# Kernel tuning notes

Measured on AMD Instinct MI355X. Metric: run time of the kernel, lower is better.

Reference implementation:

```python
import jax, jax.numpy as jnp
import numpy as np


def _lstm(x, k, r, b, return_sequences=True):
    # Keras LSTM: gate order i, f, c(g), o; sigmoid recurrent activation, tanh activation.
    # x: [B,T,D], k: [D,4H], r: [H,4H], b: [4H]
    B = x.shape[0]
    H = r.shape[0]
    xk = jnp.einsum('btd,dh->bth', x, k) + b  # precompute input projections for all steps

    def step(carry, xk_t):
        h, c = carry
        z = xk_t + h @ r
        i, f, g, o = jnp.split(z, 4, axis=-1)
        i = jax.nn.sigmoid(i)
        f = jax.nn.sigmoid(f)
        g = jnp.tanh(g)
        o = jax.nn.sigmoid(o)
        c = f * c + i * g
        h = o * jnp.tanh(c)
        return (h, c), h

    h0 = jnp.zeros((B, H), x.dtype)
    (hT, _), hs = jax.lax.scan(step, (h0, jnp.zeros_like(h0)), jnp.swapaxes(xk, 0, 1))
    if return_sequences:
        return jnp.swapaxes(hs, 0, 1)  # [B,T,H]
    return hT  # [B,H]


def _bias(h):
    # Keras unit_forget_bias=True: forget-gate bias initialized to 1
    return jnp.zeros((4 * h,), jnp.float32).at[h:2 * h].set(1.0)


def setup_inputs() -> dict:
    key = jax.random.key(0)
    ks = jax.random.split(key, 20)
    B, T, D = 128, 512, 64
    s = 0.05

    def n(k, shape):
        return jax.random.normal(k, shape, jnp.float32) * s

    inp = {"x": jax.random.normal(ks[0], (B, T, D), jnp.float32)}
    lstm_dims = [(D, 640), (640, 400), (400, 256), (256, 256)]
    i = 1
    for li, (din, h) in enumerate(lstm_dims, 1):
        inp[f"k{li}"] = n(ks[i], (din, 4 * h))
        inp[f"r{li}"] = n(ks[i + 1], (h, 4 * h))
        inp[f"b{li}"] = _bias(h)
        i += 2
    dense_dims = [(256, 512), (512, 256), (256, 128), (128, 64), (64, 16), (16, 3)]
    for li, (din, dout) in enumerate(dense_dims, 1):
        inp[f"wd{li}"] = n(ks[i], (din, dout))
        inp[f"bd{li}"] = jnp.zeros((dout,), jnp.float32)
        i += 1
    return inp


def reference(x, k1, r1, b1, k2, r2, b2, k3, r3, b3, k4, r4, b4,
              wd1, bd1, wd2, bd2, wd3, bd3, wd4, bd4, wd5, bd5, wd6, bd6):
    h = _lstm(x, k1, r1, b1, return_sequences=True)
    h = _lstm(h, k2, r2, b2, return_sequences=True)
    h = _lstm(h, k3, r3, b3, return_sequences=True)
    h = _lstm(h, k4, r4, b4, return_sequences=False)  # [B, 256]
    # Dropout layers are identity at inference (Keras call without training=True)
    h = jax.nn.relu(h @ wd1 + bd1)
    h = jax.nn.relu(h @ wd2 + bd2)
    h = jax.nn.relu(h @ wd3 + bd3)
    h = jax.nn.relu(h @ wd4 + bd4)
    h = jax.nn.relu(h @ wd5 + bd5)
    logits = h @ wd6 + bd6
    return jax.nn.softmax(logits, axis=-1)  # class_count=3 branch
```

## Files before the change

### kernel.cpp

```cpp
#include <hip/hip_runtime.h>
#include <hip/hip_cooperative_groups.h>
#include <cstdint>
#include <cstddef>

namespace cg = cooperative_groups;

typedef _Float16 f16;
typedef _Float16 h8v  __attribute__((ext_vector_type(8)));
typedef float    f32x4 __attribute__((ext_vector_type(4)));

static constexpr int BATCH  = 128;
static constexpr int TSTEPS = 512;
static constexpr int NT     = 256;

static constexpr int TB1 = 80, TB2 = 100, TB3 = 32, TB4 = 32;
static constexpr int TNB   = TB1 + TB2 + TB3 + TB4;
static constexpr int NGRID = TNB + 4;

template<int RING> struct WS {
  static constexpr size_t XT  = 0;
  static constexpr size_t H1  = XT + 512ull * 128 * 64 * 2;
  static constexpr size_t H2  = H1 + (size_t)RING * 128 * 640 * 2 + 64;
  static constexpr size_t H3  = H2 + (size_t)RING * 128 * 400 * 2 + 64;
  static constexpr size_t H4  = H3 + (size_t)RING * 128 * 256 * 2 + 64;
  static constexpr size_t PK1 = H4 + (size_t)RING * 128 * 256 * 2 + 64;
  static constexpr size_t PK2 = PK1 + (size_t)TB1 * 32 * 704  * 2;
  static constexpr size_t PK3 = PK2 + (size_t)TB2 * 16 * 1056 * 2;
  static constexpr size_t PK4 = PK3 + (size_t)TB3 * 32 * 672  * 2;
  static constexpr size_t BAR = PK4 + (size_t)TB4 * 32 * 512  * 2;
  static constexpr size_t ZERO= BAR + 8192;
  static constexpr size_t END = ZERO + 163840;
};

struct KParams {
  const float *x;
  const float *k1, *r1, *b1, *k2, *r2, *b2, *k3, *r3, *b3, *k4, *r4, *b4;
  const float *wd1, *bd1, *wd2, *bd2, *wd3, *bd3, *wd4, *bd4, *wd5, *bd5, *wd6, *bd6;
  float *out;
  char *ws;
};

__device__ __forceinline__ float sigm(float v) { return 1.f / (1.f + expf(-v)); }

__device__ __forceinline__ uint64_t c_load8(const void* p) {
  return __hip_atomic_load((const uint64_t*)p, __ATOMIC_RELAXED, __HIP_MEMORY_SCOPE_AGENT);
}
__device__ __forceinline__ void c_store8(void* p, uint64_t v) {
  __hip_atomic_store((uint64_t*)p, v, __ATOMIC_RELAXED, __HIP_MEMORY_SCOPE_AGENT);
}
__device__ __forceinline__ unsigned short c_load2(const void* p) {
  return __hip_atomic_load((const unsigned short*)p, __ATOMIC_RELAXED, __HIP_MEMORY_SCOPE_AGENT);
}
__device__ __forceinline__ unsigned u_load(const unsigned* p) {
  return __hip_atomic_load(p, __ATOMIC_RELAXED, __HIP_MEMORY_SCOPE_AGENT);
}
__device__ __forceinline__ void u_store(unsigned* p, unsigned v) {
  __hip_atomic_store(p, v, __ATOMIC_RELAXED, __HIP_MEMORY_SCOPE_AGENT);
}
__device__ __forceinline__ void acq_fence() {
  __builtin_amdgcn_fence(__ATOMIC_ACQUIRE, "agent");
}

template<int NBLK>
__device__ void control_role(unsigned* U, int first, int lidx) {
  const int tid = threadIdx.x;
  int cand = 1;
  while (cand <= TSTEPS) {
    unsigned v = (tid < NBLK) ? u_load(&U[first + tid]) : 0xFFFFFFFFu;
    if (__syncthreads_and((int)(v >= (unsigned)cand))) {
      if (tid < 16) u_store(&U[512 + tid * 64 + lidx], (unsigned)cand);
      ++cand;
    }
  }
}

__device__ void prepack_layer(const float* __restrict__ gk, const float* __restrict__ gr,
                              f16* __restrict__ pack, int DIN, int H, int NJ, int KPAD,
                              int TB, int gtid, int gstr) {
  const int KREAL = DIN + H;
  const int NGC = 4 * NJ;
  const long total = (long)TB * NGC * KPAD;
  for (long e = gtid; e < total; e += gstr) {
    const int  k   = (int)(e % KPAD);
    const long r   = e / KPAD;
    const int  n   = (int)(r % NGC);
    const int  blk = (int)(r / NGC);
    const int  g   = n / NJ, jj = n % NJ;
    const int  j   = blk * NJ + jj;
    float v = 0.f;
    if (k < DIN)        v = gk[(size_t)k * 4 * H + (size_t)g * H + j];
    else if (k < KREAL) v = gr[(size_t)(k - DIN) * 4 * H + (size_t)g * H + j];
    pack[e] = (f16)v;
  }
}

#define FETCH(PP, CC) do { \
  _Pragma("unroll") \
  for (int ii_ = 0; ii_ < C; ++ii_) { \
    const int ks_ = (CC) * C + ii_; \
    if (ks_ < KS) { \
      const int k_ = ks_ * 32 + kg; \
      _Pragma("unroll") \
      for (int m_ = 0; m_ < 2; ++m_) { \
        const int bmv_ = m_ ? bm1 : bm0; \
        uint4 v_ = make_uint4(0u, 0u, 0u, 0u); \
        if constexpr (SEQM) { \
          if (k_ < DIN)        v_ = *(const uint4*)(inP + (size_t)bmv_ * DIN + k_); \
          else if (k_ < KREAL) v_ = *(const uint4*)(inH + (size_t)bmv_ * H + (k_ - DIN)); \
        } else { \
          if (k_ < DIN) { \
            const f16* p_ = inP + (size_t)bmv_ * DIN + k_; \
            if constexpr (SEQIN) { \
              ((uint64_t*)&v_)[0] = *(const uint64_t*)p_; \
              ((uint64_t*)&v_)[1] = *(const uint64_t*)(p_ + 4); \
            } else { \
              ((uint64_t*)&v_)[0] = c_load8(p_); \
              ((uint64_t*)&v_)[1] = c_load8(p_ + 4); \
            } \
          } else if (k_ < KREAL) { \
            const f16* p_ = inH + (size_t)bmv_ * H + (k_ - DIN); \
            ((uint64_t*)&v_)[0] = c_load8(p_); \
            ((uint64_t*)&v_)[1] = c_load8(p_ + 4); \
          } \
        } \
        ab[PP][ii_][m_] = v_; \
      } \
    } \
  } \
} while (0)

#define COMPUTE(PP, CC) do { \
  _Pragma("unroll") \
  for (int ii_ = 0; ii_ < C; ++ii_) { \
    const int ks_ = (CC) * C + ii_; \
    if (ks_ < KS) { \
      const int kb_ = ks_ * 32; \
      h8v bf_[NTI]; \
      _Pragma("unroll") \
      for (int nt_ = 0; nt_ < NTI; ++nt_) \
        bf_[nt_] = *(const h8v*)(wlds + (size_t)(nt_ * 16 + l15) * WROW + kb_ + kg); \
      _Pragma("unroll") \
      for (int m_ = 0; m_ < 2; ++m_) { \
        union { uint4 u; h8v v; } af_; \
        af_.u = ab[PP][ii_][m_]; \
        _Pragma("unroll") \
        for (int nt_ = 0; nt_ < NTI; ++nt_) \
          acc[m_][nt_] = __builtin_amdgcn_mfma_f32_16x16x32_f16(af_.v, bf_[nt_], acc[m_][nt_], 0, 0, 0); \
      } \
    } \
  } \
} while (0)

#define WAITOWN do { \
  if (tid == 0) { while (rcO < t) rcO = (int)u_load(&relp[LIDX]); } \
  __syncthreads(); \
} while (0)

template<int DIN, int H, int NJ, int LIDX, bool SEQIN, int RING>
__device__ void lstm_role(int blk, int bid, const f16* lo_base, f16* ownH,
                          const f16* pack, const float* __restrict__ gbias,
                          const f16* zreg, char* smem, unsigned* U) {
  constexpr bool SEQM = (RING == TSTEPS);
  constexpr int KREAL = DIN + H;
  constexpr int KS    = (KREAL + 31) / 32;
  constexpr int KPAD  = KS * 32;
  constexpr int NGC   = 4 * NJ;
  constexpr int NTI   = NGC / 16;
  constexpr int WROW  = KPAD + 8;
  constexpr int ZROW  = 132;
  constexpr int C     = 6;
  constexpr int NC    = (KS + C - 1) / C;
  constexpr int KSX   = DIN / 32;
  constexpr int CH    = KSX / C;
  static_assert(NC <= 6, "NC");
  static_assert(CH <= NC - 1, "CH");
  static_assert(NGC % 16 == 0 && (DIN % 8) == 0 && (KREAL % 8) == 0, "geom");

  const int tid  = threadIdx.x;
  const int w    = tid >> 6, lane = tid & 63;
  const int l15  = lane & 15;
  const int kg   = (lane >> 4) * 8;
  const int bm0  = w * 32 + l15;
  const int bm1  = bm0 + 16;

  f16*   wlds = (f16*)smem;
  float* z    = (float*)(smem + (size_t)NGC * WROW * 2);

  {
    const f16* src = pack + (size_t)blk * NGC * KPAD;
    constexpr int RU = KPAD / 8;
    for (int u = tid; u < NGC * RU; u += NT) {
      const int n = u / RU, k8 = u % RU;
      *(uint4*)(wlds + (size_t)n * WROW + k8 * 8) =
          *(const uint4*)(src + (size_t)n * KPAD + k8 * 8);
    }
  }
  __syncthreads();

  constexpr int JG = NJ / 4;
  const int be  = tid / JG;
  const int g4  = tid % JG;
  const bool epi = (tid < 128 * JG);
  const int j0  = blk * NJ + g4 * 4;
  f32x4 bias4[4] = {};
  if (epi) {
    #pragma unroll
    for (int g = 0; g < 4; ++g) bias4[g] = *(const f32x4*)(gbias + (size_t)g * H + j0);
  }
  float cst[4] = {0.f, 0.f, 0.f, 0.f};

  const unsigned* relp = &U[512 + (bid & 15) * 64];
  int rcI = 0, rcO = 0, rcD = 0;
  (void)rcI; (void)rcD;

  for (int t = 0; t < TSTEPS; ++t) {
    if (tid == 0) {
      for (;;) {
        bool ok = true;
        if constexpr (CH == 0) ok = (rcO >= t);
        if constexpr (LIDX > 0) ok = ok && (rcI >= t + 1);
        if constexpr (!SEQM && LIDX < 3) ok = ok && (rcD >= t - (RING - 1));
        if (ok) break;
        if constexpr (LIDX > 0) rcI = (int)u_load(&relp[LIDX - 1]);
        if constexpr (CH == 0) rcO = (int)u_load(&relp[LIDX]);
        if constexpr (!SEQM && LIDX < 3) rcD = (int)u_load(&relp[LIDX + 1]);
      }
    }
    __syncthreads();

    const f16* inP = SEQIN ? lo_base + (size_t)t * DIN * BATCH
                           : lo_base + (size_t)(t & (RING - 1)) * DIN * BATCH;
    const f16* inH = (t == 0) ? zreg
                              : ownH + (size_t)((t - 1) & (RING - 1)) * H * BATCH;

    f32x4 acc[2][NTI];
    {
      const f32x4 zz = {0.f, 0.f, 0.f, 0.f};
      #pragma unroll
      for (int m_ = 0; m_ < 2; ++m_)
        #pragma unroll
        for (int nt_ = 0; nt_ < NTI; ++nt_) acc[m_][nt_] = zz;
    }

    uint4 ab[3][C][2];

    FETCH(0, 0);
    if constexpr (NC > 1) { if constexpr (CH == 1) WAITOWN; FETCH(1, 1); }
    if constexpr (NC > 2) { if constexpr (CH == 2) WAITOWN; FETCH(2, 2); }
    COMPUTE(0, 0);
    if constexpr (NC > 1) { if constexpr (NC > 3) { if constexpr (CH == 3) WAITOWN; FETCH(0, 3); } COMPUTE(1, 1); }
    if constexpr (NC > 2) { if constexpr (NC > 4) { if constexpr (CH == 4) WAITOWN; FETCH(1, 4); } COMPUTE(2, 2); }
    if constexpr (NC > 3) { if constexpr (NC > 5) { if constexpr (CH == 5) WAITOWN; FETCH(2, 5); } COMPUTE(0, 3); }
    if constexpr (NC > 4) COMPUTE(1, 4);
    if constexpr (NC > 5) COMPUTE(2, 5);

    #pragma unroll
    for (int m_ = 0; m_ < 2; ++m_)
      #pragma unroll
      for (int nt_ = 0; nt_ < NTI; ++nt_)
        *(f32x4*)(z + (size_t)(nt_ * 16 + l15) * ZROW + w * 32 + m_ * 16 + (lane >> 4) * 4) =
            acc[m_][nt_];
    __syncthreads();

    if (epi) {
      float vi[4], vf[4], vg[4], vo[4];
      #pragma unroll
      for (int q = 0; q < 4; ++q) {
        const int nn = g4 * 4 + q;
        vi[q] = z[(size_t)(0 * NJ + nn) * ZROW + be];
        vf[q] = z[(size_t)(1 * NJ + nn) * ZROW + be];
        vg[q] = z[(size_t)(2 * NJ + nn) * ZROW + be];
        vo[q] = z[(size_t)(3 * NJ + nn) * ZROW + be];
      }
      union { f16 h[4]; uint64_t u; } o;
      #pragma unroll
      for (int q = 0; q < 4; ++q) {
        const float ig = sigm(vi[q] + bias4[0][q]);
        const float fg = sigm(vf[q] + bias4[1][q]);
        const float gg = tanhf(vg[q] + bias4[2][q]);
        const float og = sigm(vo[q] + bias4[3][q]);
        cst[q] = fg * cst[q] + ig * gg;
        o.h[q] = (f16)(og * tanhf(cst[q]));
      }
      c_store8(ownH + (size_t)(t & (RING - 1)) * H * BATCH + (size_t)be * H + j0, o.u);
    }
    asm volatile("s_waitcnt vmcnt(0)" ::: "memory");
    __syncthreads();
    if (tid == 0) u_store(&U[bid], (unsigned)(t + 1));
  }
}
#undef FETCH
#undef COMPUTE
#undef WAITOWN

__device__ void dense_stage(const float* in, float* outb,
                            const float* __restrict__ w, const float* __restrict__ bias,
                            int din, int dout, bool relu) {
  for (int jc = threadIdx.x; jc < dout; jc += NT) {
    float s = bias[jc];
    for (int d = 0; d < din; ++d) s += in[d] * w[(size_t)d * dout + jc];
    outb[jc] = relu ? fmaxf(s, 0.f) : s;
  }
  __syncthreads();
}

constexpr size_t cmax(size_t a, size_t b) { return a > b ? a : b; }
constexpr size_t wlz(int NGC, int KPAD) {
  return (size_t)NGC * (KPAD + 8) * 2 + (size_t)NGC * 132 * 4;
}
static constexpr size_t SMEM_BYTES =
    cmax(cmax(wlz(32, 704), wlz(16, 1056)),
         cmax(cmax(wlz(32, 672), wlz(32, 512)), (size_t)4096));
static_assert(SMEM_BYTES <= 65536, "LDS");

template<int RING>
__global__ __launch_bounds__(NT, 1) void fused_kernel(KParams p) {
  using L = WS<RING>;
  cg::grid_group grid = cg::this_grid();
  __shared__ __attribute__((aligned(16))) char smem[SMEM_BYTES];

  char* ws = p.ws;
  unsigned* U = (unsigned*)(ws + L::BAR);
  const f16* zreg = (const f16*)(ws + L::ZERO);
  const int tid  = threadIdx.x;
  const int bid  = blockIdx.x;
  const int gtid = bid * NT + tid;
  const int gstr = NGRID * NT;

  prepack_layer(p.k1, p.r1, (f16*)(ws + L::PK1), 64,  640, 8, 704,  TB1, gtid, gstr);
  prepack_layer(p.k2, p.r2, (f16*)(ws + L::PK2), 640, 400, 4, 1056, TB2, gtid, gstr);
  prepack_layer(p.k3, p.r3, (f16*)(ws + L::PK3), 400, 256, 8, 672,  TB3, gtid, gstr);
  prepack_layer(p.k4, p.r4, (f16*)(ws + L::PK4), 256, 256, 8, 512,  TB4, gtid, gstr);

  {
    f16* xT = (f16*)(ws + L::XT);
    const long total = (long)TSTEPS * BATCH * 8;
    for (long u = gtid; u < total; u += gstr) {
      const int  d8 = (int)(u & 7);
      const long r  = u >> 3;
      const int  b  = (int)(r & (BATCH - 1));
      const int  t  = (int)(r >> 7);
      const float* src = p.x + ((size_t)b * TSTEPS + t) * 64 + d8 * 8;
      const float4 v0 = *(const float4*)src;
      const float4 v1 = *(const float4*)(src + 4);
      h8v o;
      o[0] = (f16)v0.x; o[1] = (f16)v0.y; o[2] = (f16)v0.z; o[3] = (f16)v0.w;
      o[4] = (f16)v1.x; o[5] = (f16)v1.y; o[6] = (f16)v1.z; o[7] = (f16)v1.w;
      *(h8v*)(xT + ((size_t)t * BATCH + b) * 64 + d8 * 8) = o;
    }
  }

  grid.sync();
  acq_fence();

  constexpr int TRB2 = TB1, TRB3 = TB1 + TB2, TRB4 = TB1 + TB2 + TB3;
  if (bid >= TNB) {
    const int l = bid - TNB;
    if (l == 0)      control_role<TB1>(U, 0,    0);
    else if (l == 1) control_role<TB2>(U, TRB2, 1);
    else if (l == 2) control_role<TB3>(U, TRB3, 2);
    else             control_role<TB4>(U, TRB4, 3);
  } else if (bid < TRB2) {
    lstm_role< 64, 640, 8, 0, true , RING>(bid, bid, (const f16*)(ws + L::XT),
        (f16*)(ws + L::H1), (const f16*)(ws + L::PK1), p.b1, zreg, smem, U);
  } else if (bid < TRB3) {
    lstm_role<640, 400, 4, 1, false, RING>(bid - TRB2, bid, (const f16*)(ws + L::H1),
        (f16*)(ws + L::H2), (const f16*)(ws + L::PK2), p.b2, zreg, smem, U);
  } else if (bid < TRB4) {
    lstm_role<400, 256, 8, 2, false, RING>(bid - TRB3, bid, (const f16*)(ws + L::H2),
        (f16*)(ws + L::H3), (const f16*)(ws + L::PK3), p.b3, zreg, smem, U);
  } else {
    lstm_role<256, 256, 8, 3, false, RING>(bid - TRB4, bid, (const f16*)(ws + L::H3),
        (f16*)(ws + L::H4), (const f16*)(ws + L::PK4), p.b4, zreg, smem, U);
  }

  if (bid < BATCH) {
    if (tid == 0) {
      const unsigned* relp = &U[512 + (bid & 15) * 64];
      while ((int)u_load(&relp[3]) < TSTEPS) {}
    }
    __syncthreads();
    const int b = bid;
    float* A = (float*)smem;
    float* B = (float*)smem + 512;
    const f16* h4 = (const f16*)(ws + L::H4)
                  + (size_t)((TSTEPS - 1) & (RING - 1)) * 256 * BATCH + (size_t)b * 256;
    for (int d = tid; d < 256; d += NT) {
      union { unsigned short u; f16 h; } cc;
      cc.u = c_load2(h4 + d);
      A[d] = (float)cc.h;
    }
    __syncthreads();
    dense_stage(A, B, p.wd1, p.bd1, 256, 512, true);
    dense_stage(B, A, p.wd2, p.bd2, 512, 256, true);
    dense_stage(A, B, p.wd3, p.bd3, 256, 128, true);
    dense_stage(B, A, p.wd4, p.bd4, 128, 64,  true);
    dense_stage(A, B, p.wd5, p.bd5, 64,  16,  true);
    dense_stage(B, A, p.wd6, p.bd6, 16,  3,   false);
    if (tid == 0) {
      float z0 = A[0], z1 = A[1], z2 = A[2];
      float m  = fmaxf(fmaxf(z0, z1), z2);
      float e0 = expf(z0 - m), e1 = expf(z1 - m), e2 = expf(z2 - m);
      float s  = e0 + e1 + e2;
      p.out[b * 3 + 0] = e0 / s;
      p.out[b * 3 + 1] = e1 / s;
      p.out[b * 3 + 2] = e2 / s;
    }
  }
}

extern "C" void kernel_launch(void* const* d_in, const int* in_sizes, int n_in,
                              void* d_out, int out_size, void* d_ws, size_t ws_size,
                              hipStream_t stream) {
  (void)in_sizes; (void)n_in; (void)out_size;
  KParams prm;
  prm.x  = (const float*)d_in[0];
  prm.k1 = (const float*)d_in[1];  prm.r1 = (const float*)d_in[2];  prm.b1 = (const float*)d_in[3];
  prm.k2 = (const float*)d_in[4];  prm.r2 = (const float*)d_in[5];  prm.b2 = (const float*)d_in[6];
  prm.k3 = (const float*)d_in[7];  prm.r3 = (const float*)d_in[8];  prm.b3 = (const float*)d_in[9];
  prm.k4 = (const float*)d_in[10]; prm.r4 = (const float*)d_in[11]; prm.b4 = (const float*)d_in[12];
  prm.wd1 = (const float*)d_in[13]; prm.bd1 = (const float*)d_in[14];
  prm.wd2 = (const float*)d_in[15]; prm.bd2 = (const float*)d_in[16];
  prm.wd3 = (const float*)d_in[17]; prm.bd3 = (const float*)d_in[18];
  prm.wd4 = (const float*)d_in[19]; prm.bd4 = (const float*)d_in[20];
  prm.wd5 = (const float*)d_in[21]; prm.bd5 = (const float*)d_in[22];
  prm.wd6 = (const float*)d_in[23]; prm.bd6 = (const float*)d_in[24];
  prm.out = (float*)d_out;
  prm.ws  = (char*)d_ws;

  const bool big = ws_size >= WS<TSTEPS>::END;
  const size_t bar_off = big ? WS<TSTEPS>::BAR : WS<4>::BAR;
  hipMemsetAsync((char*)d_ws + bar_off, 0, 8192 + 163840, stream);

  void* args[] = { &prm };
  if (big) {
    hipLaunchCooperativeKernel((void*)fused_kernel<TSTEPS>, dim3(NGRID), dim3(NT),
                               args, 0, stream);
  } else {
    hipLaunchCooperativeKernel((void*)fused_kernel<4>, dim3(NGRID), dim3(NT),
                               args, 0, stream);
  }
}
```

Measured before the change: 5.003 ms.

## Replace block-level barriers with per-wavefront progress counters in LSTM pipeline

```diff
diff --git a/kernel.cpp b/kernel.cpp
--- a/kernel.cpp
+++ b/kernel.cpp
@@ -63,12 +63,14 @@
 
 template<int NBLK>
 __device__ void control_role(unsigned* U, int first, int lidx) {
-  const int tid = threadIdx.x;
+  const int w = threadIdx.x >> 6, lane = threadIdx.x & 63;
   int cand = 1;
   while (cand <= TSTEPS) {
-    unsigned v = (tid < NBLK) ? u_load(&U[first + tid]) : 0xFFFFFFFFu;
-    if (__syncthreads_and((int)(v >= (unsigned)cand))) {
-      if (tid < 16) u_store(&U[512 + tid * 64 + lidx], (unsigned)cand);
+    unsigned v0 = (lane < NBLK)      ? u_load(&U[4 * (first + lane) + w])      : 0xFFFFFFFFu;
+    unsigned v1 = (lane + 64 < NBLK) ? u_load(&U[4 * (first + lane + 64) + w]) : 0xFFFFFFFFu;
+    unsigned v = v0 < v1 ? v0 : v1;
+    if (__all((int)(v >= (unsigned)cand))) {
+      if (lane < 16) u_store(&U[1024 + lane * 64 + lidx * 4 + w], (unsigned)cand);
       ++cand;
     }
   }
@@ -152,8 +154,10 @@
 } while (0)
 
 #define WAITOWN do { \
-  if (tid == 0) { while (rcO < t) rcO = (int)u_load(&relp[LIDX]); } \
-  __syncthreads(); \
+  bool c_ = (lane != 0) || (rcO >= t); \
+  while (!__all((int)c_)) { \
+    if (!c_) { rcO = (int)u_load(&relp[LIDX * 4 + w]); c_ = (rcO >= t); } \
+  } \
 } while (0)
 
 template<int DIN, int H, int NJ, int LIDX, bool SEQIN, int RING>
@@ -197,11 +201,11 @@
   }
   __syncthreads();
 
-  constexpr int JG = NJ / 4;
-  const int be  = tid / JG;
-  const int g4  = tid % JG;
-  const bool epi = (tid < 128 * JG);
-  const int j0  = blk * NJ + g4 * 4;
+  constexpr int JW = NJ / 4;
+  const int be  = 32 * w + lane / JW;
+  const int jg  = lane % JW;
+  const bool epi = (lane < 32 * JW);
+  const int j0  = blk * NJ + jg * 4;
   f32x4 bias4[4] = {};
   if (epi) {
     #pragma unroll
@@ -209,24 +213,30 @@
   }
   float cst[4] = {0.f, 0.f, 0.f, 0.f};
 
-  const unsigned* relp = &U[512 + (bid & 15) * 64];
+  const unsigned* relp = &U[1024 + (bid & 15) * 64];
   int rcI = 0, rcO = 0, rcD = 0;
   (void)rcI; (void)rcD;
 
   for (int t = 0; t < TSTEPS; ++t) {
-    if (tid == 0) {
-      for (;;) {
-        bool ok = true;
-        if constexpr (CH == 0) ok = (rcO >= t);
-        if constexpr (LIDX > 0) ok = ok && (rcI >= t + 1);
-        if constexpr (!SEQM && LIDX < 3) ok = ok && (rcD >= t - (RING - 1));
-        if (ok) break;
-        if constexpr (LIDX > 0) rcI = (int)u_load(&relp[LIDX - 1]);
-        if constexpr (CH == 0) rcO = (int)u_load(&relp[LIDX]);
-        if constexpr (!SEQM && LIDX < 3) rcD = (int)u_load(&relp[LIDX + 1]);
+    {
+      bool c = true;
+      if constexpr (LIDX > 0) { if (lane == 0) c = (rcI >= t + 1); }
+      if constexpr (CH == 0)  { if (lane == 1) c = (rcO >= t); }
+      if constexpr (!SEQM && LIDX < 3) { if (lane == 2) c = (rcD >= t - (RING - 1)); }
+      while (!__all((int)c)) {
+        if (!c) {
+          if constexpr (LIDX > 0) {
+            if (lane == 0) { rcI = (int)u_load(&relp[(LIDX - 1) * 4 + w]); c = (rcI >= t + 1); }
+          }
+          if constexpr (CH == 0) {
+            if (lane == 1) { rcO = (int)u_load(&relp[LIDX * 4 + w]); c = (rcO >= t); }
+          }
+          if constexpr (!SEQM && LIDX < 3) {
+            if (lane == 2) { rcD = (int)u_load(&relp[(LIDX + 1) * 4 + w]); c = (rcD >= t - (RING - 1)); }
+          }
+        }
       }
     }
-    __syncthreads();
 
     const f16* inP = SEQIN ? lo_base + (size_t)t * DIN * BATCH
                            : lo_base + (size_t)(t & (RING - 1)) * DIN * BATCH;
@@ -260,13 +270,12 @@
       for (int nt_ = 0; nt_ < NTI; ++nt_)
         *(f32x4*)(z + (size_t)(nt_ * 16 + l15) * ZROW + w * 32 + m_ * 16 + (lane >> 4) * 4) =
             acc[m_][nt_];
-    __syncthreads();
 
     if (epi) {
       float vi[4], vf[4], vg[4], vo[4];
       #pragma unroll
       for (int q = 0; q < 4; ++q) {
-        const int nn = g4 * 4 + q;
+        const int nn = jg * 4 + q;
         vi[q] = z[(size_t)(0 * NJ + nn) * ZROW + be];
         vf[q] = z[(size_t)(1 * NJ + nn) * ZROW + be];
         vg[q] = z[(size_t)(2 * NJ + nn) * ZROW + be];
@@ -285,8 +294,7 @@
       c_store8(ownH + (size_t)(t & (RING - 1)) * H * BATCH + (size_t)be * H + j0, o.u);
     }
     asm volatile("s_waitcnt vmcnt(0)" ::: "memory");
-    __syncthreads();
-    if (tid == 0) u_store(&U[bid], (unsigned)(t + 1));
+    if (lane == 0) u_store(&U[4 * bid + w], (unsigned)(t + 1));
   }
 }
 #undef FETCH
@@ -375,9 +383,15 @@
   }
 
   if (bid < BATCH) {
-    if (tid == 0) {
-      const unsigned* relp = &U[512 + (bid & 15) * 64];
-      while ((int)u_load(&relp[3]) < TSTEPS) {}
+    if (tid < 64) {
+      bool c = (tid >= 4);
+      int rc = 0;
+      while (!__all((int)c)) {
+        if (!c) {
+          rc = (int)u_load(&U[1024 + (bid & 15) * 64 + 3 * 4 + tid]);
+          c = (rc >= TSTEPS);
+        }
+      }
     }
     __syncthreads();
     const int b = bid;
```

Result: faster. 4.854 ms (-3.0%).
